# Kernel tuning notes

Hardware: AMD Instinct MI355X
Metric: run time of the kernel (lower is better)

Reference implementation:

```python
import jax, jax.numpy as jnp
import numpy as np

D_MODEL = 1024
NUM_HEADS = 16
HEAD_DIM = D_MODEL // NUM_HEADS
SCALE = HEAD_DIM ** -0.5


def setup_inputs() -> dict:
    key = jax.random.key(0)
    ks = jax.random.split(key, 8)
    B, Nq, Nk = 2, 2048, 2048
    s = D_MODEL ** -0.5  # init scale for weights
    return {
        "query": jax.random.normal(ks[0], (B, Nq, D_MODEL), jnp.float32),
        "key": jax.random.normal(ks[1], (B, Nk, D_MODEL), jnp.float32),
        "value": jax.random.normal(ks[2], (B, Nk, D_MODEL), jnp.float32),
        "Wq": jax.random.normal(ks[3], (D_MODEL, D_MODEL), jnp.float32) * s,
        "Wk": jax.random.normal(ks[4], (D_MODEL, D_MODEL), jnp.float32) * s,
        "Wv": jax.random.normal(ks[5], (D_MODEL, D_MODEL), jnp.float32) * s,
        "Wo": jax.random.normal(ks[6], (D_MODEL, D_MODEL), jnp.float32) * s,
        "bo": jnp.zeros((D_MODEL,), jnp.float32),
    }


def reference(query, key, value, Wq, Wk, Wv, Wo, bo):
    B, Nq, C = query.shape
    Nk = key.shape[1]
    H, Dh = NUM_HEADS, HEAD_DIM
    # projections (torch Linear: x @ W.T)
    q = (query @ Wq.T).reshape(B, Nq, H, Dh).transpose(0, 2, 1, 3)  # [B,H,Nq,Dh]
    k = (key @ Wk.T).reshape(B, Nk, H, Dh).transpose(0, 2, 1, 3)    # [B,H,Nk,Dh]
    v = (value @ Wv.T).reshape(B, Nk, H, Dh).transpose(0, 2, 1, 3)  # [B,H,Nk,Dh]
    # explicit attention: QK^T * scale -> softmax -> @V
    sim = jnp.einsum("bhqd,bhkd->bhqk", q, k) * SCALE
    attn = jax.nn.softmax(sim, axis=-1)
    out = jnp.einsum("bhqk,bhkd->bhqd", attn, v)
    out = out.transpose(0, 2, 1, 3).reshape(B, Nq, C)
    return out @ Wo.T + bo
```

## Files before the change

### kernel.cpp

```cpp
#include <hip/hip_runtime.h>
#include <hip/hip_bf16.h>

typedef __attribute__((ext_vector_type(8))) short short8;
typedef __attribute__((ext_vector_type(4))) short short4v;
typedef __attribute__((ext_vector_type(4))) float f32x4;

#define DEVFN static __device__ __forceinline__

constexpr int D_MODEL = 1024;
constexpr int NH  = 16;
constexpr int DH  = 64;
constexpr int SEQ = 2048;
constexpr float SCALE_LOG2E = 0.125f * 1.44269504088896341f;

DEVFN short bf16s(float f) {
  __hip_bfloat16 h = __float2bfloat16(f);
  short s; __builtin_memcpy(&s, &h, 2);
  return s;
}

DEVFN float fast_exp2(float x) {
#if __has_builtin(__builtin_amdgcn_exp2f)
  return __builtin_amdgcn_exp2f(x);
#else
  return exp2f(x);
#endif
}

DEVFN void wait_vm0() { asm volatile("s_waitcnt vmcnt(0)" ::: "memory"); }

DEVFN void gload_lds16(const void* g, void* l) {
  __builtin_amdgcn_global_load_lds(
      (const __attribute__((address_space(1))) unsigned int*)g,
      (__attribute__((address_space(3))) unsigned int*)l, 16, 0, 0);
}

__global__ __launch_bounds__(256)
void castk(const float* __restrict__ src, short* __restrict__ dst, int n8, float scale)
{
  int i = blockIdx.x * blockDim.x + threadIdx.x;
  if (i >= n8) return;
  const float4 a = *(const float4*)(src + (size_t)i*8);
  const float4 b = *(const float4*)(src + (size_t)i*8 + 4);
  short8 v;
  v[0]=bf16s(a.x*scale); v[1]=bf16s(a.y*scale); v[2]=bf16s(a.z*scale); v[3]=bf16s(a.w*scale);
  v[4]=bf16s(b.x*scale); v[5]=bf16s(b.y*scale); v[6]=bf16s(b.z*scale); v[7]=bf16s(b.w*scale);
  *(short8*)(dst + (size_t)i*8) = v;
}

__global__ __launch_bounds__(256, 3)
void qkv_gemm(const float* __restrict__ Aq, const float* __restrict__ Ak,
              const float* __restrict__ Av,
              const short* __restrict__ Wq, const short* __restrict__ Wk,
              const short* __restrict__ Wv,
              short* __restrict__ Qp, short* __restrict__ Kp, short* __restrict__ Vp)
{
  __shared__ char smem[2*24576];

  const int id  = blockIdx.x;
  const int swz = (id & 7)*96 + (id >> 3);
  const int z   = swz >> 8;
  const int rr  = swz & 255;
  const int m0  = (rr >> 3) * 128, n0 = (rr & 7) * 128;

  const float* Af = (z == 0) ? Aq : (z == 1) ? Ak : Av;
  const short* Wb = (z == 0) ? Wq : (z == 1) ? Wk : Wv;
  short* Cp       = (z == 0) ? Qp : (z == 1) ? Kp : Vp;

  const int tid = threadIdx.x, lane = tid & 63, w = tid >> 6;
  const int wr = w >> 1, wc = w & 1;
  const int l15 = lane & 15, l4 = lane >> 4;

  f32x4 acc[4][4];
  #pragma unroll
  for (int i = 0; i < 4; ++i)
    #pragma unroll
    for (int j = 0; j < 4; ++j) acc[i][j] = f32x4{0.f,0.f,0.f,0.f};

  auto stage = [&](char* buf, int k0) {
    #pragma unroll
    for (int p = 0; p < 4; ++p) {
      const int off = (w*4 + p)*1024 + lane*16;
      const int row = off >> 7;
      const int cb  = (off & 127) ^ ((row & 7) << 4);
      gload_lds16(Af + (size_t)(m0 + row)*D_MODEL + k0 + (cb >> 2),
                  buf + (w*4 + p)*1024);
    }
    #pragma unroll
    for (int p = 0; p < 2; ++p) {
      const int off = (w*2 + p)*1024 + lane*16;
      const int row = off >> 6;
      const int cb  = (off & 63) ^ ((row & 3) << 4);
      gload_lds16(Wb + (size_t)(n0 + row)*D_MODEL + k0 + (cb >> 1),
                  buf + 16384 + (w*2 + p)*1024);
    }
  };

  stage(smem, 0);
  wait_vm0();
  __builtin_amdgcn_s_barrier();

  for (int kt = 0; kt < D_MODEL/32; ++kt) {
    char* buf = smem + (kt & 1)*24576;
    if (kt + 1 < D_MODEL/32) stage(smem + ((kt+1) & 1)*24576, (kt+1)*32);

    char* AsB = buf; char* WsB = buf + 16384;
    short8 af[4], bf[4];
    #pragma unroll
    for (int fi = 0; fi < 4; ++fi) {
      const int row = wr*64 + fi*16 + l15;
      const int s_ = (row & 7) << 4;
      f32x4 x0 = *(const f32x4*)(AsB + row*128 + ((l4*32) ^ s_));
      f32x4 x1 = *(const f32x4*)(AsB + row*128 + ((l4*32 + 16) ^ s_));
      short8 a;
      a[0]=bf16s(x0[0]); a[1]=bf16s(x0[1]); a[2]=bf16s(x0[2]); a[3]=bf16s(x0[3]);
      a[4]=bf16s(x1[0]); a[5]=bf16s(x1[1]); a[6]=bf16s(x1[2]); a[7]=bf16s(x1[3]);
      af[fi] = a;
    }
    #pragma unroll
    for (int fj = 0; fj < 4; ++fj) {
      const int row = wc*64 + fj*16 + l15;
      bf[fj] = *(const short8*)(WsB + row*64 + ((l4*16) ^ ((row & 3) << 4)));
    }
    #pragma unroll
    for (int fi = 0; fi < 4; ++fi)
      #pragma unroll
      for (int fj = 0; fj < 4; ++fj)
        acc[fi][fj] = __builtin_amdgcn_mfma_f32_16x16x32_bf16(af[fi], bf[fj], acc[fi][fj], 0, 0, 0);

    wait_vm0();
    __builtin_amdgcn_s_barrier();
  }

  #pragma unroll
  for (int fi = 0; fi < 4; ++fi)
    #pragma unroll
    for (int fj = 0; fj < 4; ++fj)
      #pragma unroll
      for (int r = 0; r < 4; ++r) {
        const int m = m0 + wr*64 + fi*16 + l4*4 + r;
        const int j = n0 + wc*64 + fj*16 + l15;
        const int b = m >> 11, n = m & (SEQ-1);
        const int h = j >> 6,  d = j & 63;
        const short v = bf16s(acc[fi][fj][r]);
        if (z == 2)
          Cp[((size_t)(b*NH + h)*DH + d)*SEQ + n] = v;
        else
          Cp[(((size_t)(b*NH + h)*SEQ + n) << 6) + d] = v;
      }
}

__global__ __launch_bounds__(256, 4)
void gemm_out(const short* __restrict__ A, const short* __restrict__ Wb,
              const float* __restrict__ bias, float* __restrict__ Cp)
{
  __shared__ char smem[2*12288];

  const int id  = blockIdx.x;
  const int swz = (id & 7)*64 + (id >> 3);
  const int m0  = (swz >> 4) * 128, n0 = (swz & 15) * 64;

  const int tid = threadIdx.x, lane = tid & 63, w = tid >> 6;
  const int wr = w >> 1, wc = w & 1;
  const int l15 = lane & 15, l4 = lane >> 4;

  f32x4 acc[4][2];
  #pragma unroll
  for (int i = 0; i < 4; ++i)
    #pragma unroll
    for (int j = 0; j < 2; ++j) acc[i][j] = f32x4{0.f,0.f,0.f,0.f};

  auto stage = [&](char* buf, int k0) {
    #pragma unroll
    for (int p = 0; p < 2; ++p) {
      const int off = (w*2 + p)*1024 + lane*16;
      const int row = off >> 6;
      const int cb  = (off & 63) ^ ((row & 3) << 4);
      gload_lds16(A + (size_t)(m0 + row)*D_MODEL + k0 + (cb >> 1),
                  buf + (w*2 + p)*1024);
    }
    {
      const int off = w*1024 + lane*16;
      const int row = off >> 6;
      const int cb  = (off & 63) ^ ((row & 3) << 4);
      gload_lds16(Wb + (size_t)(n0 + row)*D_MODEL + k0 + (cb >> 1),
                  buf + 8192 + w*1024);
    }
  };

  stage(smem, 0);
  wait_vm0();
  __builtin_amdgcn_s_barrier();

  for (int kt = 0; kt < D_MODEL/32; ++kt) {
    char* buf = smem + (kt & 1)*12288;
    if (kt + 1 < D_MODEL/32) stage(smem + ((kt+1) & 1)*12288, (kt+1)*32);

    char* AsB = buf; char* WsB = buf + 8192;
    short8 af[4], bf[2];
    #pragma unroll
    for (int fi = 0; fi < 4; ++fi) {
      const int row = wr*64 + fi*16 + l15;
      af[fi] = *(const short8*)(AsB + row*64 + ((l4*16) ^ ((row & 3) << 4)));
    }
    #pragma unroll
    for (int fj = 0; fj < 2; ++fj) {
      const int row = wc*32 + fj*16 + l15;
      bf[fj] = *(const short8*)(WsB + row*64 + ((l4*16) ^ ((row & 3) << 4)));
    }
    #pragma unroll
    for (int fi = 0; fi < 4; ++fi)
      #pragma unroll
      for (int fj = 0; fj < 2; ++fj)
        acc[fi][fj] = __builtin_amdgcn_mfma_f32_16x16x32_bf16(af[fi], bf[fj], acc[fi][fj], 0, 0, 0);

    wait_vm0();
    __builtin_amdgcn_s_barrier();
  }

  float bj[2];
  #pragma unroll
  for (int fj = 0; fj < 2; ++fj) bj[fj] = bias[n0 + wc*32 + fj*16 + l15];
  #pragma unroll
  for (int fi = 0; fi < 4; ++fi)
    #pragma unroll
    for (int fj = 0; fj < 2; ++fj)
      #pragma unroll
      for (int r = 0; r < 4; ++r) {
        const int m = m0 + wr*64 + fi*16 + l4*4 + r;
        const int j = n0 + wc*32 + fj*16 + l15;
        Cp[(size_t)m*D_MODEL + j] = acc[fi][fj][r] + bj[fj];
      }
}

__global__ __launch_bounds__(512, 2)
void attn_fwd(const short* __restrict__ Qh, const short* __restrict__ Kh,
              const short* __restrict__ Vt, __hip_bfloat16* __restrict__ AO)
{
  __shared__ char smem[2*16384 + 16384];
  char* PsAll = smem + 32768;

  const int id  = blockIdx.x;
  const int swz = (id & 7)*64 + (id >> 3);
  const int bh  = swz >> 4;
  const int q0  = (swz & 15) * 128;

  const int tid = threadIdx.x, lane = tid & 63, w = tid >> 6;
  const int l15 = lane & 15, l4 = lane >> 4;
  const int b = bh >> 4, h = bh & 15;
  const size_t base = (size_t)bh * SEQ * DH;
  char* PsB = PsAll + w * 2048;

  const short* Kg = Kh + base;
  const short* Vg = Vt + base;

  short8 qf[2];
  #pragma unroll
  for (int kc = 0; kc < 2; ++kc)
    qf[kc] = *(const short8*)(Qh + base + (size_t)(q0 + w*16 + l15)*DH + kc*32 + l4*8);

  float m = -1e30f, l = 0.f;
  f32x4 o[4];
  #pragma unroll
  for (int fj = 0; fj < 4; ++fj) o[fj] = f32x4{0.f,0.f,0.f,0.f};

  const int soff = w*1024 + lane*16;
  const int srow = soff >> 7;
  const int scb  = (soff & 127) ^ ((srow & 7) << 4);

  auto stage = [&](char* buf, int kt) {
    gload_lds16(Kg + (size_t)(kt*64 + srow)*DH + (scb >> 1), buf + w*1024);
    gload_lds16(Vg + (size_t)srow*SEQ + kt*64 + (scb >> 1),  buf + 8192 + w*1024);
  };

  stage(smem, 0);
  wait_vm0();
  __builtin_amdgcn_s_barrier();

  constexpr int NT = SEQ/64;
  for (int kt = 0; kt < NT; ++kt) {
    char* KsB = smem + (kt & 1)*16384;
    char* VsB = KsB + 8192;
    if (kt + 1 < NT) stage(smem + ((kt+1) & 1)*16384, kt + 1);

    f32x4 s[4];
    #pragma unroll
    for (int fj = 0; fj < 4; ++fj) s[fj] = f32x4{0.f,0.f,0.f,0.f};
    #pragma unroll
    for (int kc = 0; kc < 2; ++kc)
      #pragma unroll
      for (int fj = 0; fj < 4; ++fj) {
        const int row = fj*16 + l15;
        short8 kf = *(const short8*)(KsB + ((row*128 + (kc*32 + l4*8)*2) ^ ((row & 7) << 4)));
        s[fj] = __builtin_amdgcn_mfma_f32_16x16x32_bf16(kf, qf[kc], s[fj], 0, 0, 0);
      }

    float pmax = s[0][0];
    #pragma unroll
    for (int fj = 0; fj < 4; ++fj)
      #pragma unroll
      for (int r = 0; r < 4; ++r) pmax = fmaxf(pmax, s[fj][r]);
    pmax = fmaxf(pmax, __shfl_xor(pmax, 16, 64));
    pmax = fmaxf(pmax, __shfl_xor(pmax, 32, 64));
    const float mn = fmaxf(m, pmax);
    const float al = fast_exp2(m - mn);
    m = mn;
    float rs = 0.f;
    #pragma unroll
    for (int fj = 0; fj < 4; ++fj)
      #pragma unroll
      for (int r = 0; r < 4; ++r) {
        s[fj][r] = fast_exp2(s[fj][r] - m);
        rs += s[fj][r];
      }
    rs += __shfl_xor(rs, 16, 64);
    rs += __shfl_xor(rs, 32, 64);
    l = l * al + rs;

    #pragma unroll
    for (int fj = 0; fj < 4; ++fj) {
      short4v c;
      c[0]=bf16s(s[fj][0]); c[1]=bf16s(s[fj][1]); c[2]=bf16s(s[fj][2]); c[3]=bf16s(s[fj][3]);
      const int byo = (l15*128 + (fj*16 + l4*4)*2) ^ ((l15 & 7) << 4);
      *(short4v*)(PsB + byo) = c;
    }

    float alr[4];
    #pragma unroll
    for (int r = 0; r < 4; ++r) alr[r] = __shfl(al, l4*4 + r, 64);
    #pragma unroll
    for (int fj = 0; fj < 4; ++fj)
      #pragma unroll
      for (int r = 0; r < 4; ++r) o[fj][r] *= alr[r];

    #pragma unroll
    for (int kc = 0; kc < 2; ++kc) {
      const int pb = (l15*128 + (kc*32 + l4*8)*2) ^ ((l15 & 7) << 4);
      short8 pa = *(const short8*)(PsB + pb);
      #pragma unroll
      for (int fj = 0; fj < 4; ++fj) {
        const int row = fj*16 + l15;
        short8 vf = *(const short8*)(VsB + ((row*128 + (kc*32 + l4*8)*2) ^ ((row & 7) << 4)));
        o[fj] = __builtin_amdgcn_mfma_f32_16x16x32_bf16(pa, vf, o[fj], 0, 0, 0);
      }
    }

    wait_vm0();
    __builtin_amdgcn_s_barrier();
  }

  const float inv = 1.0f / l;
  float ivr[4];
  #pragma unroll
  for (int r = 0; r < 4; ++r) ivr[r] = __shfl(inv, l4*4 + r, 64);
  #pragma unroll
  for (int fj = 0; fj < 4; ++fj)
    #pragma unroll
    for (int r = 0; r < 4; ++r) {
      const int n = q0 + w*16 + l4*4 + r;
      const int d = h*64 + fj*16 + l15;
      AO[(size_t)(b*SEQ + n)*D_MODEL + d] = __float2bfloat16(o[fj][r] * ivr[r]);
    }
}

extern "C" void kernel_launch(void* const* d_in, const int* in_sizes, int n_in,
                              void* d_out, int out_size, void* d_ws, size_t ws_size,
                              hipStream_t stream)
{
  const float* query = (const float*)d_in[0];
  const float* key_  = (const float*)d_in[1];
  const float* value = (const float*)d_in[2];
  const float* Wq = (const float*)d_in[3];
  const float* Wk = (const float*)d_in[4];
  const float* Wv = (const float*)d_in[5];
  const float* Wo = (const float*)d_in[6];
  const float* bo = (const float*)d_in[7];

  char* wsb = (char*)d_ws;
  short* Qp  = (short*)(wsb);
  short* Kp  = (short*)(wsb + (8u  << 20));
  short* Vp  = (short*)(wsb + (16u << 20));
  short* Wqb = (short*)(wsb + (24u << 20));
  short* Wkb = (short*)(wsb + (26u << 20));
  short* Wvb = (short*)(wsb + (28u << 20));
  short* Ao  = (short*)(wsb + (24u << 20));
  short* Wob = (short*)(wsb);

  const int nW = D_MODEL*D_MODEL/8;
  castk<<<nW/256, 256, 0, stream>>>(Wq, Wqb, nW, SCALE_LOG2E);
  castk<<<nW/256, 256, 0, stream>>>(Wk, Wkb, nW, 1.f);
  castk<<<nW/256, 256, 0, stream>>>(Wv, Wvb, nW, 1.f);

  qkv_gemm<<<768, 256, 0, stream>>>(query, key_, value, Wqb, Wkb, Wvb, Qp, Kp, Vp);
  attn_fwd<<<512, 512, 0, stream>>>(Qp, Kp, Vp, (__hip_bfloat16*)Ao);

  castk<<<nW/256, 256, 0, stream>>>(Wo, Wob, nW, 1.f);
  gemm_out<<<512, 256, 0, stream>>>(Ao, Wob, bo, (float*)d_out);
}
```

Baseline: 242.7 us.

## Triple-buffer LDS pipelines in GEMMs and attention, skip unchanged softmax rescale

Switches the QKV GEMM, output GEMM and attention kernels from double- to triple-buffered LDS staging. Each iteration now waits with a partial vmcnt, so the next-but-one tile stays in flight during compute, and the trailing barrier per iteration is gone. Attention also skips the running-max rescale of the output accumulators when no lane's max increased. Launch-bounds occupancy hints change as well. The cost is more LDS per block, which may lower occupancy (qkv_gemm hint drops to 2), and the vmcnt counts must match the loads issued per stage exactly.

```diff
diff --git a/kernel.cpp b/kernel.cpp
--- a/kernel.cpp
+++ b/kernel.cpp
@@ -27,7 +27,7 @@
 #endif
 }
 
-DEVFN void wait_vm0() { asm volatile("s_waitcnt vmcnt(0)" ::: "memory"); }
+DEVFN int inc3(int x) { return x == 2 ? 0 : x + 1; }
 
 DEVFN void gload_lds16(const void* g, void* l) {
   __builtin_amdgcn_global_load_lds(
@@ -48,14 +48,14 @@
   *(short8*)(dst + (size_t)i*8) = v;
 }
 
-__global__ __launch_bounds__(256, 3)
+__global__ __launch_bounds__(256, 2)
 void qkv_gemm(const float* __restrict__ Aq, const float* __restrict__ Ak,
               const float* __restrict__ Av,
               const short* __restrict__ Wq, const short* __restrict__ Wk,
               const short* __restrict__ Wv,
               short* __restrict__ Qp, short* __restrict__ Kp, short* __restrict__ Vp)
 {
-  __shared__ char smem[2*24576];
+  __shared__ char smem[3*24576];
 
   const int id  = blockIdx.x;
   const int swz = (id & 7)*96 + (id >> 3);
@@ -77,7 +77,8 @@
     #pragma unroll
     for (int j = 0; j < 4; ++j) acc[i][j] = f32x4{0.f,0.f,0.f,0.f};
 
-  auto stage = [&](char* buf, int k0) {
+  auto stage = [&](int sb, int k0) {
+    char* buf = smem + sb*24576;
     #pragma unroll
     for (int p = 0; p < 4; ++p) {
       const int off = (w*4 + p)*1024 + lane*16;
@@ -96,15 +97,9 @@
     }
   };
 
-  stage(smem, 0);
-  wait_vm0();
-  __builtin_amdgcn_s_barrier();
-
-  for (int kt = 0; kt < D_MODEL/32; ++kt) {
-    char* buf = smem + (kt & 1)*24576;
-    if (kt + 1 < D_MODEL/32) stage(smem + ((kt+1) & 1)*24576, (kt+1)*32);
-
-    char* AsB = buf; char* WsB = buf + 16384;
+  auto compute = [&](int cb_) {
+    char* AsB = smem + cb_*24576;
+    char* WsB = AsB + 16384;
     short8 af[4], bf[4];
     #pragma unroll
     for (int fi = 0; fi < 4; ++fi) {
@@ -127,10 +122,24 @@
       #pragma unroll
       for (int fj = 0; fj < 4; ++fj)
         acc[fi][fj] = __builtin_amdgcn_mfma_f32_16x16x32_bf16(af[fi], bf[fj], acc[fi][fj], 0, 0, 0);
-
-    wait_vm0();
+  };
+
+  constexpr int NIT = D_MODEL/32;
+  stage(0, 0);
+  stage(1, 32);
+  int cur = 0, nxt = 2;
+  for (int kt = 0; kt < NIT-1; ++kt) {
+    asm volatile("s_waitcnt vmcnt(6)" ::: "memory");
     __builtin_amdgcn_s_barrier();
+    __builtin_amdgcn_sched_barrier(0);
+    if (kt + 2 < NIT) stage(nxt, (kt+2)*32);
+    compute(cur);
+    cur = inc3(cur); nxt = inc3(nxt);
   }
+  asm volatile("s_waitcnt vmcnt(0)" ::: "memory");
+  __builtin_amdgcn_s_barrier();
+  __builtin_amdgcn_sched_barrier(0);
+  compute(cur);
 
   #pragma unroll
   for (int fi = 0; fi < 4; ++fi)
@@ -154,7 +163,7 @@
 void gemm_out(const short* __restrict__ A, const short* __restrict__ Wb,
               const float* __restrict__ bias, float* __restrict__ Cp)
 {
-  __shared__ char smem[2*12288];
+  __shared__ char smem[3*12288];
 
   const int id  = blockIdx.x;
   const int swz = (id & 7)*64 + (id >> 3);
@@ -170,7 +179,8 @@
     #pragma unroll
     for (int j = 0; j < 2; ++j) acc[i][j] = f32x4{0.f,0.f,0.f,0.f};
 
-  auto stage = [&](char* buf, int k0) {
+  auto stage = [&](int sb, int k0) {
+    char* buf = smem + sb*12288;
     #pragma unroll
     for (int p = 0; p < 2; ++p) {
       const int off = (w*2 + p)*1024 + lane*16;
@@ -188,15 +198,9 @@
     }
   };
 
-  stage(smem, 0);
-  wait_vm0();
-  __builtin_amdgcn_s_barrier();
-
-  for (int kt = 0; kt < D_MODEL/32; ++kt) {
-    char* buf = smem + (kt & 1)*12288;
-    if (kt + 1 < D_MODEL/32) stage(smem + ((kt+1) & 1)*12288, (kt+1)*32);
-
-    char* AsB = buf; char* WsB = buf + 8192;
+  auto compute = [&](int cb_) {
+    char* AsB = smem + cb_*12288;
+    char* WsB = AsB + 8192;
     short8 af[4], bf[2];
     #pragma unroll
     for (int fi = 0; fi < 4; ++fi) {
@@ -213,10 +217,24 @@
       #pragma unroll
       for (int fj = 0; fj < 2; ++fj)
         acc[fi][fj] = __builtin_amdgcn_mfma_f32_16x16x32_bf16(af[fi], bf[fj], acc[fi][fj], 0, 0, 0);
-
-    wait_vm0();
+  };
+
+  constexpr int NIT = D_MODEL/32;
+  stage(0, 0);
+  stage(1, 32);
+  int cur = 0, nxt = 2;
+  for (int kt = 0; kt < NIT-1; ++kt) {
+    asm volatile("s_waitcnt vmcnt(3)" ::: "memory");
     __builtin_amdgcn_s_barrier();
+    __builtin_amdgcn_sched_barrier(0);
+    if (kt + 2 < NIT) stage(nxt, (kt+2)*32);
+    compute(cur);
+    cur = inc3(cur); nxt = inc3(nxt);
   }
+  asm volatile("s_waitcnt vmcnt(0)" ::: "memory");
+  __builtin_amdgcn_s_barrier();
+  __builtin_amdgcn_sched_barrier(0);
+  compute(cur);
 
   float bj[2];
   #pragma unroll
@@ -233,12 +251,12 @@
       }
 }
 
-__global__ __launch_bounds__(512, 2)
+__global__ __launch_bounds__(512, 4)
 void attn_fwd(const short* __restrict__ Qh, const short* __restrict__ Kh,
               const short* __restrict__ Vt, __hip_bfloat16* __restrict__ AO)
 {
-  __shared__ char smem[2*16384 + 16384];
-  char* PsAll = smem + 32768;
+  __shared__ char smem[3*16384 + 16384];
+  char* PsAll = smem + 49152;
 
   const int id  = blockIdx.x;
   const int swz = (id & 7)*64 + (id >> 3);
@@ -268,20 +286,15 @@
   const int srow = soff >> 7;
   const int scb  = (soff & 127) ^ ((srow & 7) << 4);
 
-  auto stage = [&](char* buf, int kt) {
+  auto stage = [&](int sb, int kt) {
+    char* buf = smem + sb*16384;
     gload_lds16(Kg + (size_t)(kt*64 + srow)*DH + (scb >> 1), buf + w*1024);
     gload_lds16(Vg + (size_t)srow*SEQ + kt*64 + (scb >> 1),  buf + 8192 + w*1024);
   };
 
-  stage(smem, 0);
-  wait_vm0();
-  __builtin_amdgcn_s_barrier();
-
-  constexpr int NT = SEQ/64;
-  for (int kt = 0; kt < NT; ++kt) {
-    char* KsB = smem + (kt & 1)*16384;
+  auto compute = [&](int cb_) {
+    char* KsB = smem + cb_*16384;
     char* VsB = KsB + 8192;
-    if (kt + 1 < NT) stage(smem + ((kt+1) & 1)*16384, kt + 1);
 
     f32x4 s[4];
     #pragma unroll
@@ -302,9 +315,21 @@
       for (int r = 0; r < 4; ++r) pmax = fmaxf(pmax, s[fj][r]);
     pmax = fmaxf(pmax, __shfl_xor(pmax, 16, 64));
     pmax = fmaxf(pmax, __shfl_xor(pmax, 32, 64));
-    const float mn = fmaxf(m, pmax);
-    const float al = fast_exp2(m - mn);
-    m = mn;
+
+    if (!__all(pmax <= m)) {
+      const float mn = fmaxf(m, pmax);
+      const float al = fast_exp2(m - mn);
+      m = mn;
+      l *= al;
+      float alr[4];
+      #pragma unroll
+      for (int r = 0; r < 4; ++r) alr[r] = __shfl(al, l4*4 + r, 64);
+      #pragma unroll
+      for (int fj = 0; fj < 4; ++fj)
+        #pragma unroll
+        for (int r = 0; r < 4; ++r) o[fj][r] *= alr[r];
+    }
+
     float rs = 0.f;
     #pragma unroll
     for (int fj = 0; fj < 4; ++fj)
@@ -315,7 +340,7 @@
       }
     rs += __shfl_xor(rs, 16, 64);
     rs += __shfl_xor(rs, 32, 64);
-    l = l * al + rs;
+    l += rs;
 
     #pragma unroll
     for (int fj = 0; fj < 4; ++fj) {
@@ -325,14 +350,6 @@
       *(short4v*)(PsB + byo) = c;
     }
 
-    float alr[4];
-    #pragma unroll
-    for (int r = 0; r < 4; ++r) alr[r] = __shfl(al, l4*4 + r, 64);
-    #pragma unroll
-    for (int fj = 0; fj < 4; ++fj)
-      #pragma unroll
-      for (int r = 0; r < 4; ++r) o[fj][r] *= alr[r];
-
     #pragma unroll
     for (int kc = 0; kc < 2; ++kc) {
       const int pb = (l15*128 + (kc*32 + l4*8)*2) ^ ((l15 & 7) << 4);
@@ -344,10 +361,24 @@
         o[fj] = __builtin_amdgcn_mfma_f32_16x16x32_bf16(pa, vf, o[fj], 0, 0, 0);
       }
     }
-
-    wait_vm0();
+  };
+
+  constexpr int NT = SEQ/64;
+  stage(0, 0);
+  stage(1, 1);
+  int cur = 0, nxt = 2;
+  for (int kt = 0; kt < NT-1; ++kt) {
+    asm volatile("s_waitcnt vmcnt(2)" ::: "memory");
     __builtin_amdgcn_s_barrier();
+    __builtin_amdgcn_sched_barrier(0);
+    if (kt + 2 < NT) stage(nxt, kt + 2);
+    compute(cur);
+    cur = inc3(cur); nxt = inc3(nxt);
   }
+  asm volatile("s_waitcnt vmcnt(0)" ::: "memory");
+  __builtin_amdgcn_s_barrier();
+  __builtin_amdgcn_sched_barrier(0);
+  compute(cur);
 
   const float inv = 1.0f / l;
   float ivr[4];
```

New measurement: 238.3 us. Within noise of the previous version (-1.8%).
